# Performance work log

Measured on AMD Instinct MI355X. Metric: run time of the kernel, lower is better.

The kernel has to match this reference:

```python
import jax, jax.numpy as jnp
import numpy as np

B, H, W, C = 32, 32, 32, 256
AD, RR = 8, 16
DN = ('NHWC', 'HWIO', 'NHWC')


def _conv(a, w, dil=1, groups=1):
    return jax.lax.conv_general_dilated(a, w, (1, 1), 'SAME', rhs_dilation=(dil, dil),
                                        dimension_numbers=DN, feature_group_count=groups)


def _branch(a, w1, b1, dw, pw, b3, wd, bd):
    # (Conv1x1 + SeparableConv3x3 + DilatedConv3x3), each sigmoid-activated, averaged
    y1 = jax.nn.sigmoid(_conv(a, w1) + b1)
    y3 = jax.nn.sigmoid(_conv(_conv(a, dw, groups=a.shape[-1]), pw) + b3)  # depthwise (no bias) -> pointwise
    yd = jax.nn.sigmoid(_conv(a, wd, dil=2) + bd)
    return (y1 + y3 + yd) / 3.0


def setup_inputs() -> dict:
    key = jax.random.key(0)
    ks = iter(jax.random.split(key, 64))
    nrm = lambda shape, s=0.05: jax.random.normal(next(ks), shape, jnp.float32) * s
    d = {'x': jax.random.normal(next(ks), (B, H, W, C), jnp.float32)}
    for p in ('cc', 'ch', 'cw'):
        d[p + '1_w'] = nrm((1, 1, C, 1)); d[p + '1_b'] = jnp.zeros((1,), jnp.float32)
        d[p + '3_dw'] = nrm((3, 3, 1, C)); d[p + '3_pw'] = nrm((1, 1, C, 1)); d[p + '3_b'] = jnp.zeros((1,), jnp.float32)
        d[p + 'd_w'] = nrm((3, 3, C, 1)); d[p + 'd_b'] = jnp.zeros((1,), jnp.float32)
    d['branch_w'] = jax.random.uniform(next(ks), (3,), jnp.float32, -0.05, 0.05)
    d['d1_w'] = nrm((C, RR)); d['d1_b'] = jnp.zeros((RR,), jnp.float32)
    d['d2_w'] = nrm((RR, 1)); d['d2_b'] = jnp.zeros((1,), jnp.float32)
    for p in ('q', 'k', 'v'):
        d[p + '_w'] = nrm((1, 1, 3, AD)); d[p + '_b'] = jnp.zeros((AD,), jnp.float32)
    d['o_w'] = nrm((1, 1, AD, 1)); d['o_b'] = jnp.zeros((1,), jnp.float32)
    d['gamma'] = jnp.ones((H, W, C), jnp.float32)
    d['beta'] = jnp.zeros((H, W, C), jnp.float32)
    return d


def reference(x, cc1_w, cc1_b, cc3_dw, cc3_pw, cc3_b, ccd_w, ccd_b,
              ch1_w, ch1_b, ch3_dw, ch3_pw, ch3_b, chd_w, chd_b,
              cw1_w, cw1_b, cw3_dw, cw3_pw, cw3_b, cwd_w, cwd_b,
              branch_w, d1_w, d1_b, d2_w, d2_b,
              q_w, q_b, k_w, k_b, v_w, v_b, o_w, o_b, gamma, beta):
    Bx, Hx, Wx, Cx = x.shape
    # global SE context: GAP -> Dense(relu) -> Dense(sigmoid) -> broadcast over H,W
    g = jnp.mean(x, axis=(1, 2), keepdims=True)                       # [B,1,1,C]
    g = jax.nn.relu(g @ d1_w + d1_b)
    g = jax.nn.sigmoid(g @ d2_w + d2_b)                               # [B,1,1,1]
    # channel branch: mean over H,W -> convs over [B,1,1,C] -> scalar gate
    ca = _branch(jnp.mean(x, axis=(1, 2), keepdims=True), cc1_w, cc1_b, cc3_dw, cc3_pw, cc3_b, ccd_w, ccd_b)  # [B,1,1,1]
    x_c = x * ca
    # height branch: mean over W -> [B,1,H,C] -> convs -> [B,1,H,1] -> gate per-H
    ha_in = jnp.transpose(jnp.mean(x, axis=2, keepdims=True), (0, 2, 1, 3))
    ha = _branch(ha_in, ch1_w, ch1_b, ch3_dw, ch3_pw, ch3_b, chd_w, chd_b)
    x_h = x * jnp.transpose(ha, (0, 2, 1, 3))                         # [B,H,1,1] broadcast
    # width branch: mean over H -> [B,1,W,C] -> convs -> [B,1,W,1] -> gate per-W
    wa = _branch(jnp.mean(x, axis=1, keepdims=True), cw1_w, cw1_b, cw3_dw, cw3_pw, cw3_b, cwd_w, cwd_b)
    x_w = x * wa
    bw = jax.nn.softmax(branch_w)
    combined = bw[0] * x_c + bw[1] * x_h + bw[2] * x_w
    # small self-attention over the 3 channel-mean maps
    maps = jnp.concatenate([jnp.mean(x_c, axis=-1, keepdims=True),
                            jnp.mean(x_h, axis=-1, keepdims=True),
                            jnp.mean(x_w, axis=-1, keepdims=True)], axis=-1)  # [B,H,W,3]
    Q = (jnp.einsum('bhwc,co->bhwo', maps, q_w[0, 0]) + q_b).reshape(Bx, Hx * Wx, AD)
    K = (jnp.einsum('bhwc,co->bhwo', maps, k_w[0, 0]) + k_b).reshape(Bx, Hx * Wx, AD)
    V = (jnp.einsum('bhwc,co->bhwo', maps, v_w[0, 0]) + v_b).reshape(Bx, Hx * Wx, AD)
    att = jax.nn.softmax(jnp.einsum('bnd,bmd->bnm', Q, K) / jnp.sqrt(jnp.float32(AD)), axis=-1)
    ao = jnp.einsum('bnm,bmd->bnd', att, V).reshape(Bx, Hx, Wx, AD)
    cross = jax.nn.sigmoid(jnp.einsum('bhwd,do->bhwo', ao, o_w[0, 0]) + o_b)  # [B,H,W,1]
    y = combined * cross * g + x
    # LayerNorm over (H,W,C) per sample, keras eps=1e-3
    mu = jnp.mean(y, axis=(1, 2, 3), keepdims=True)
    var = jnp.mean((y - mu) ** 2, axis=(1, 2, 3), keepdims=True)
    return (y - mu) / jnp.sqrt(var + 1e-3) * gamma + beta
```

## Files before the change

kernel.cpp:

```cpp
#include <hip/hip_runtime.h>


#define B_   32
#define H_   32
#define W_   32
#define C_   256
#define N_   1024
#define HWC_ (32*32*256)

#define OFF_XW    0
#define OFF_XH    262144
#define OFF_MC    524288
#define OFF_M2    557056
#define OFF_T     589824
#define OFF_HA    622592
#define OFF_WA    623616
#define OFF_CA    624640
#define OFF_G     624672
#define OFF_CST   624704
#define OFF_LNP   624736
#define WS_FLOATS 628832

#if __has_builtin(__builtin_amdgcn_exp2f)
#define EXP2F(x) __builtin_amdgcn_exp2f(x)
#else
#define EXP2F(x) exp2f(x)
#endif

__device__ __forceinline__ float sigm_(float v){ return 1.f/(1.f + __expf(-v)); }
__device__ __forceinline__ float dot4_(float4 a, float4 b){
  return a.x*b.x + a.y*b.y + a.z*b.z + a.w*b.w;
}

__global__ __launch_bounds__(256) void kA(const float* __restrict__ x, float* __restrict__ ws){
  __shared__ float4 sl4[256];
  const int blk = blockIdx.x, b = blk >> 5, h = blk & 31;
  const int tid = threadIdx.x, lane = tid & 63, wv = tid >> 6;
  const float* xp = x + (size_t)blk*(W_*C_);
  float4 v[8];
  #pragma unroll
  for (int k = 0; k < 8; ++k) v[k] = ((const float4*)xp)[tid + k*256];
  #pragma unroll
  for (int k = 0; k < 8; ++k){
    float s = v[k].x + v[k].y + v[k].z + v[k].w;
    float q = v[k].x*v[k].x + v[k].y*v[k].y + v[k].z*v[k].z + v[k].w*v[k].w;
    #pragma unroll
    for (int d = 1; d < 64; d <<= 1){ s += __shfl_xor(s, d); q += __shfl_xor(q, d); }
    if (lane == 0){
      const int w = k*4 + wv;
      ws[OFF_MC + b*N_ + h*W_ + w] = s * (1.f/C_);
      ws[OFF_M2 + b*N_ + h*W_ + w] = q;
    }
  }
  float4 a = v[0];
  #pragma unroll
  for (int k = 1; k < 8; ++k){ a.x += v[k].x; a.y += v[k].y; a.z += v[k].z; a.w += v[k].w; }
  sl4[tid] = a;
  __syncthreads();
  if (tid < 64){
    const float4 p0 = sl4[tid], p1 = sl4[tid+64], p2 = sl4[tid+128], p3 = sl4[tid+192];
    float4 o;
    o.x = (p0.x+p1.x+p2.x+p3.x)*(1.f/W_);
    o.y = (p0.y+p1.y+p2.y+p3.y)*(1.f/W_);
    o.z = (p0.z+p1.z+p2.z+p3.z)*(1.f/W_);
    o.w = (p0.w+p1.w+p2.w+p3.w)*(1.f/W_);
    ((float4*)(ws + OFF_XW + (size_t)blk*C_))[tid] = o;
  }
}

__global__ __launch_bounds__(256) void kB(const float* __restrict__ x, float* __restrict__ ws){
  __shared__ float4 sl4[256];
  const int blk = blockIdx.x, b = blk >> 5, w = blk & 31;
  const int tid = threadIdx.x;
  const int hh = tid >> 6, c4 = (tid & 63)*4;
  const float* xp = x + (size_t)b*HWC_ + (size_t)w*C_ + c4;
  float4 acc = {0.f,0.f,0.f,0.f};
  #pragma unroll
  for (int hb = 0; hb < 8; ++hb){
    const int h = hb*4 + hh;
    const float4 v = *(const float4*)(xp + (size_t)h*(W_*C_));
    acc.x += v.x; acc.y += v.y; acc.z += v.z; acc.w += v.w;
  }
  sl4[tid] = acc;
  __syncthreads();
  if (tid < 64){
    const float4 a = sl4[tid], b2 = sl4[tid+64], c = sl4[tid+128], d = sl4[tid+192];
    float4 o;
    o.x = (a.x+b2.x+c.x+d.x)*(1.f/H_);
    o.y = (a.y+b2.y+c.y+d.y)*(1.f/H_);
    o.z = (a.z+b2.z+c.z+d.z)*(1.f/H_);
    o.w = (a.w+b2.w+c.w+d.w)*(1.f/H_);
    *(float4*)&ws[OFF_XH + (b*W_ + w)*C_ + tid*4] = o;
  }
}

__global__ __launch_bounds__(256) void kC(float* __restrict__ ws,
  const float* __restrict__ cc1_w, const float* __restrict__ cc1_b, const float* __restrict__ cc3_dw,
  const float* __restrict__ cc3_pw, const float* __restrict__ cc3_b, const float* __restrict__ ccd_w, const float* __restrict__ ccd_b,
  const float* __restrict__ ch1_w, const float* __restrict__ ch1_b, const float* __restrict__ ch3_dw,
  const float* __restrict__ ch3_pw, const float* __restrict__ ch3_b, const float* __restrict__ chd_w, const float* __restrict__ chd_b,
  const float* __restrict__ cw1_w, const float* __restrict__ cw1_b, const float* __restrict__ cw3_dw,
  const float* __restrict__ cw3_pw, const float* __restrict__ cw3_b, const float* __restrict__ cwd_w, const float* __restrict__ cwd_b,
  const float* __restrict__ branch_w, const float* __restrict__ d1_w, const float* __restrict__ d1_b,
  const float* __restrict__ d2_w, const float* __restrict__ d2_b,
  const float* __restrict__ q_w, const float* __restrict__ q_b, const float* __restrict__ k_w, const float* __restrict__ k_b,
  const float* __restrict__ v_w, const float* __restrict__ v_b, const float* __restrict__ o_w, const float* __restrict__ o_b)
{
  const int b = blockIdx.x, y = blockIdx.y;
  const int tid = threadIdx.x, lane = tid & 63, wv = tid >> 6;

  if (y < 16){
    const int prof = y >> 3;
    const int h = ((y & 7) << 2) | wv;
    const float* P  = ws + (prof ? OFF_XH : OFF_XW) + b*(32*C_);
    const float* w1 = prof ? cw1_w  : ch1_w;
    const float* b1 = prof ? cw1_b  : ch1_b;
    const float* dw = prof ? cw3_dw : ch3_dw;
    const float* pw = prof ? cw3_pw : ch3_pw;
    const float* b3 = prof ? cw3_b  : ch3_b;
    const float* wd = prof ? cwd_w  : chd_w;
    const float* bd = prof ? cwd_b  : chd_b;
    const int c4 = lane*4;
    const float4 z4 = {0.f,0.f,0.f,0.f};
    const float4 r0  = *(const float4*)(P + h*C_ + c4);
    const float4 rm1 = (h > 0)  ? *(const float4*)(P + (h-1)*C_ + c4) : z4;
    const float4 rp1 = (h < 31) ? *(const float4*)(P + (h+1)*C_ + c4) : z4;
    const float4 rm2 = (h > 1)  ? *(const float4*)(P + (h-2)*C_ + c4) : z4;
    const float4 rp2 = (h < 30) ? *(const float4*)(P + (h+2)*C_ + c4) : z4;
    const float4 w1q = *(const float4*)(w1 + c4);
    const float4 d3  = *(const float4*)(dw + 3*C_ + c4);
    const float4 d4  = *(const float4*)(dw + 4*C_ + c4);
    const float4 d5  = *(const float4*)(dw + 5*C_ + c4);
    const float4 pwq = *(const float4*)(pw + c4);
    const float4 g3  = *(const float4*)(wd + 3*C_ + c4);
    const float4 g4  = *(const float4*)(wd + 4*C_ + c4);
    const float4 g5  = *(const float4*)(wd + 5*C_ + c4);
    float s1 = dot4_(r0, w1q);
    float4 dv;
    dv.x = rm1.x*d3.x + r0.x*d4.x + rp1.x*d5.x;
    dv.y = rm1.y*d3.y + r0.y*d4.y + rp1.y*d5.y;
    dv.z = rm1.z*d3.z + r0.z*d4.z + rp1.z*d5.z;
    dv.w = rm1.w*d3.w + r0.w*d4.w + rp1.w*d5.w;
    float s3 = dot4_(dv, pwq);
    float sd = (rm2.x*g3.x + r0.x*g4.x + rp2.x*g5.x)
             + (rm2.y*g3.y + r0.y*g4.y + rp2.y*g5.y)
             + (rm2.z*g3.z + r0.z*g4.z + rp2.z*g5.z)
             + (rm2.w*g3.w + r0.w*g4.w + rp2.w*g5.w);
    #pragma unroll
    for (int d = 1; d < 64; d <<= 1){ s1 += __shfl_xor(s1,d); s3 += __shfl_xor(s3,d); sd += __shfl_xor(sd,d); }
    if (lane == 0)
      ws[(prof ? OFF_WA : OFF_HA) + b*32 + h] =
          (sigm_(s1 + b1[0]) + sigm_(s3 + b3[0]) + sigm_(sd + bd[0])) * (1.f/3.f);
    return;
  }

  __shared__ float gvec[C_];
  { float s = 0.f;
    const float* P = ws + OFF_XW + b*(32*C_);
    #pragma unroll
    for (int h = 0; h < H_; ++h) s += P[h*C_ + tid];
    gvec[tid] = s * (1.f/H_); }
  __syncthreads();

  if (wv == 0){
    float s1 = 0.f, s3 = 0.f, sd = 0.f;
    #pragma unroll
    for (int k = 0; k < 4; ++k){
      const int c = lane + k*64;
      const float v = gvec[c];
      s1 = fmaf(v, cc1_w[c], s1);
      s3 = fmaf(v*cc3_dw[4*C_+c], cc3_pw[c], s3);
      sd = fmaf(v, ccd_w[4*C_+c], sd);
    }
    #pragma unroll
    for (int d = 1; d < 64; d <<= 1){ s1 += __shfl_xor(s1,d); s3 += __shfl_xor(s3,d); sd += __shfl_xor(sd,d); }
    if (lane == 0)
      ws[OFF_CA + b] = (sigm_(s1+cc1_b[0]) + sigm_(s3+cc3_b[0]) + sigm_(sd+ccd_b[0])) * (1.f/3.f);
  } else if (wv == 1){
    const int r16 = lane & 15, cg = lane >> 4;
    float s = 0.f;
    #pragma unroll
    for (int i = 0; i < 64; ++i){
      const int c = cg*64 + i;
      s = fmaf(gvec[c], d1_w[c*16 + r16], s);
    }
    s += __shfl_xor(s, 16); s += __shfl_xor(s, 32);
    float t = fmaxf(s + d1_b[r16], 0.f) * d2_w[r16];
    t += __shfl_xor(t, 1); t += __shfl_xor(t, 2); t += __shfl_xor(t, 4); t += __shfl_xor(t, 8);
    if (lane == 0) ws[OFF_G + b] = sigm_(t + d2_b[0]);
  } else if (wv == 2 && b == 0){
    if (lane < 16){
      const int i = lane >> 2, j = lane & 3;
      float s = 0.f;
      #pragma unroll
      for (int d = 0; d < 8; ++d){
        const float qv = (i < 3) ? q_w[i*8+d] : q_b[d];
        const float kv = (j < 3) ? k_w[j*8+d] : k_b[d];
        s = fmaf(qv, kv, s);
      }
      ws[OFF_CST + i*4 + j] = s * 0.51010305898f;
    } else if (lane < 19){
      const int i = lane - 16;
      float s = 0.f;
      #pragma unroll
      for (int d = 0; d < 8; ++d) s = fmaf(v_w[i*8+d], o_w[d], s);
      ws[OFF_CST + lane] = s;
    } else if (lane == 19){
      float s = o_b[0];
      #pragma unroll
      for (int d = 0; d < 8; ++d) s = fmaf(v_b[d], o_w[d], s);
      ws[OFF_CST + 19] = s;
    } else if (lane == 20){
      const float b0 = branch_w[0], b1 = branch_w[1], b2 = branch_w[2];
      const float mx = fmaxf(b0, fmaxf(b1, b2));
      const float e0 = __expf(b0-mx), e1 = __expf(b1-mx), e2 = __expf(b2-mx);
      const float inv = 1.f/(e0+e1+e2);
      ws[OFF_CST+20] = e0*inv; ws[OFF_CST+21] = e1*inv; ws[OFF_CST+22] = e2*inv;
      ws[OFF_CST+23] = 0.f;
    }
  }
}

__global__ __launch_bounds__(256, 4) void kD(float* __restrict__ ws){
  __shared__ __align__(16) float mcs[N_];
  __shared__ __align__(16) float qs [N_];
  __shared__ float ha_s[32], wa_s[32], cst[24], sc[2], red[8];
  const int blk = blockIdx.x, b = blk >> 6, rblk = blk & 63;
  const int tid = threadIdx.x, lane = tid & 63, wv = tid >> 6;
  const int r = tid >> 4, sub = tid & 15;
  const int sh = sub >> 3, sw = sub & 7;
  const int n = rblk*16 + r;
  const int hn = n >> 5, wn = n & 31;

  const float4 v  = ((const float4*)(ws + OFF_MC + b*N_))[tid];
  const float m2v = ws[OFF_M2 + b*N_ + n];
  const float mcn = ws[OFF_MC + b*N_ + n];
  if (tid < 32){ ha_s[tid] = ws[OFF_HA + b*32 + tid]; wa_s[tid] = ws[OFF_WA + b*32 + tid]; }
  else if (tid >= 64 && tid < 88) cst[tid-64] = ws[OFF_CST + (tid-64)];
  else if (tid == 96){ sc[0] = ws[OFF_CA + b]; sc[1] = ws[OFF_G + b]; }
  *(float4*)&mcs[tid*4] = v;
  __syncthreads();

  const float ca = sc[0], gg = sc[1];
  {
    const int hm0 = tid >> 3;
    const int wm0 = (tid*4) & 31;
    const float base = ca*cst[16] + cst[17]*ha_s[hm0];
    float4 q;
    q.x = v.x * (base + cst[18]*wa_s[wm0+0]);
    q.y = v.y * (base + cst[18]*wa_s[wm0+1]);
    q.z = v.z * (base + cst[18]*wa_s[wm0+2]);
    q.w = v.w * (base + cst[18]*wa_s[wm0+3]);
    *(float4*)&qs[tid*4] = q;
  }
  __syncthreads();

  const float u0 = mcn*ca, u1 = mcn*ha_s[hn], u2 = mcn*wa_s[wn];
  const float p0 = u0*cst[0] + u1*cst[4] + u2*cst[8]  + cst[12];
  const float p1 = u0*cst[1] + u1*cst[5] + u2*cst[9]  + cst[13];
  const float p2 = u0*cst[2] + u1*cst[6] + u2*cst[10] + cst[14];
  const float p3 = u0*cst[3] + u1*cst[7] + u2*cst[11] + cst[15];
  const float pc = p0 * ca;

  const float4 w4 = *(const float4*)&wa_s[4*sw];
  float4 pw;
  pw.x = p2*w4.x; pw.y = p2*w4.y; pw.z = p2*w4.z; pw.w = p2*w4.w;

  float Z = 0.f, ACC = 0.f;
  #pragma unroll
  for (int i = 0; i < 16; ++i){
    const int hm = sh*16 + i;
    const float th = fmaf(p1, ha_s[hm], pc);
    const float4 m4 = *(const float4*)&mcs[hm*32 + 4*sw];
    const float4 q4 = *(const float4*)&qs [hm*32 + 4*sw];
    { const float ee = EXP2F(fmaf(m4.x, th + pw.x, p3)); Z += ee; ACC = fmaf(ee, q4.x, ACC); }
    { const float ee = EXP2F(fmaf(m4.y, th + pw.y, p3)); Z += ee; ACC = fmaf(ee, q4.y, ACC); }
    { const float ee = EXP2F(fmaf(m4.z, th + pw.z, p3)); Z += ee; ACC = fmaf(ee, q4.z, ACC); }
    { const float ee = EXP2F(fmaf(m4.w, th + pw.w, p3)); Z += ee; ACC = fmaf(ee, q4.w, ACC); }
  }
  #pragma unroll
  for (int d = 1; d < 16; d <<= 1){
    Z   += __shfl_xor(Z, d);
    ACC += __shfl_xor(ACC, d);
  }

  float t1 = 0.f, t2 = 0.f;
  if (sub == 0){
    const float dot = ACC / Z + cst[19];
    const float cross = 1.f / (1.f + __expf(-dot));
    const float S = cst[20]*ca + cst[21]*ha_s[hn] + cst[22]*wa_s[wn];
    const float T = fmaf(S*cross, gg, 1.f);
    ws[OFF_T + b*N_ + n] = T;
    t1 = T * mcn * (float)C_;
    t2 = T * T * m2v;
  }
  #pragma unroll
  for (int d = 1; d < 64; d <<= 1){ t1 += __shfl_xor(t1,d); t2 += __shfl_xor(t2,d); }
  if (lane == 0){ red[wv] = t1; red[4+wv] = t2; }
  __syncthreads();
  if (tid == 0){
    ws[OFF_LNP + (b*64 + rblk)*2 + 0] = red[0]+red[1]+red[2]+red[3];
    ws[OFF_LNP + (b*64 + rblk)*2 + 1] = red[4]+red[5]+red[6]+red[7];
  }
}

__global__ __launch_bounds__(256) void kF(const float* __restrict__ x, const float* __restrict__ gamma,
                                          const float* __restrict__ beta, const float* __restrict__ ws,
                                          float* __restrict__ out){
  const int blk = blockIdx.x, b = blk >> 5, h = blk & 31;
  const int tid = threadIdx.x;
  __shared__ float a1s[32];
  __shared__ float mu_r[2];
  if (tid < 64){
    float s1 = ws[OFF_LNP + (b*64 + tid)*2 + 0];
    float s2 = ws[OFF_LNP + (b*64 + tid)*2 + 1];
    #pragma unroll
    for (int d = 1; d < 64; d <<= 1){ s1 += __shfl_xor(s1, d); s2 += __shfl_xor(s2, d); }
    if (tid == 0){
      const float mu  = s1 * (1.f/HWC_);
      const float var = s2 * (1.f/HWC_) - mu*mu;
      const float rstd = rsqrtf(var + 1e-3f);
      mu_r[0] = mu * rstd; mu_r[1] = rstd;
    }
  }
  __syncthreads();
  if (tid < 32) a1s[tid] = ws[OFF_T + b*N_ + h*32 + tid] * mu_r[1];
  __syncthreads();
  const float murstd = mu_r[0];
  const size_t base = (size_t)(b*H_ + h)*(W_*C_);
  const float4* xp = (const float4*)(x + base);
  const float4* gp = (const float4*)(gamma + (size_t)h*(W_*C_));
  const float4* bp = (const float4*)(beta  + (size_t)h*(W_*C_));
  float4* op = (float4*)(out + base);
  #pragma unroll
  for (int k = 0; k < 8; ++k){
    const int f = tid + k*256;
    const float a1 = a1s[f >> 6];
    const float4 xv = xp[f], gv = gp[f], bv = bp[f];
    float4 o;
    o.x = fmaf(fmaf(xv.x, a1, -murstd), gv.x, bv.x);
    o.y = fmaf(fmaf(xv.y, a1, -murstd), gv.y, bv.y);
    o.z = fmaf(fmaf(xv.z, a1, -murstd), gv.z, bv.z);
    o.w = fmaf(fmaf(xv.w, a1, -murstd), gv.w, bv.w);
    op[f] = o;
  }
}

extern "C" void kernel_launch(void* const* d_in, const int* in_sizes, int n_in,
                              void* d_out, int out_size, void* d_ws, size_t ws_size,
                              hipStream_t stream){
  (void)in_sizes; (void)n_in; (void)out_size;
  if (ws_size < (size_t)WS_FLOATS * sizeof(float)) return;
  const float* x      = (const float*)d_in[0];
  const float* cc1_w  = (const float*)d_in[1];
  const float* cc1_b  = (const float*)d_in[2];
  const float* cc3_dw = (const float*)d_in[3];
  const float* cc3_pw = (const float*)d_in[4];
  const float* cc3_b  = (const float*)d_in[5];
  const float* ccd_w  = (const float*)d_in[6];
  const float* ccd_b  = (const float*)d_in[7];
  const float* ch1_w  = (const float*)d_in[8];
  const float* ch1_b  = (const float*)d_in[9];
  const float* ch3_dw = (const float*)d_in[10];
  const float* ch3_pw = (const float*)d_in[11];
  const float* ch3_b  = (const float*)d_in[12];
  const float* chd_w  = (const float*)d_in[13];
  const float* chd_b  = (const float*)d_in[14];
  const float* cw1_w  = (const float*)d_in[15];
  const float* cw1_b  = (const float*)d_in[16];
  const float* cw3_dw = (const float*)d_in[17];
  const float* cw3_pw = (const float*)d_in[18];
  const float* cw3_b  = (const float*)d_in[19];
  const float* cwd_w  = (const float*)d_in[20];
  const float* cwd_b  = (const float*)d_in[21];
  const float* branch_w = (const float*)d_in[22];
  const float* d1_w   = (const float*)d_in[23];
  const float* d1_b   = (const float*)d_in[24];
  const float* d2_w   = (const float*)d_in[25];
  const float* d2_b   = (const float*)d_in[26];
  const float* q_w    = (const float*)d_in[27];
  const float* q_b    = (const float*)d_in[28];
  const float* k_w    = (const float*)d_in[29];
  const float* k_b    = (const float*)d_in[30];
  const float* v_w    = (const float*)d_in[31];
  const float* v_b    = (const float*)d_in[32];
  const float* o_w    = (const float*)d_in[33];
  const float* o_b    = (const float*)d_in[34];
  const float* gamma  = (const float*)d_in[35];
  const float* beta   = (const float*)d_in[36];
  float* ws = (float*)d_ws;
  float* out = (float*)d_out;

  kA<<<dim3(1024), dim3(256), 0, stream>>>(x, ws);
  kB<<<dim3(1024), dim3(256), 0, stream>>>(x, ws);
  kC<<<dim3(B_, 17), dim3(256), 0, stream>>>(ws,
      cc1_w, cc1_b, cc3_dw, cc3_pw, cc3_b, ccd_w, ccd_b,
      ch1_w, ch1_b, ch3_dw, ch3_pw, ch3_b, chd_w, chd_b,
      cw1_w, cw1_b, cw3_dw, cw3_pw, cw3_b, cwd_w, cwd_b,
      branch_w, d1_w, d1_b, d2_w, d2_b,
      q_w, q_b, k_w, k_b, v_w, v_b, o_w, o_b);
  kD<<<dim3(B_*64), dim3(256), 0, stream>>>(ws);
  kF<<<dim3(B_*H_), dim3(256), 0, stream>>>(x, gamma, beta, ws, out);
}
```

Measured before the change: 46.24 us.

## Fuse row and column reductions into one pass over x with partial sums

Replaces separate row-mean and column-mean kernels, which each read all of x, with one kernel that reads each row of x once and accumulates per-group column partial sums into workspace. A small second kernel then sums the eight partials per column. This removes a full second read of the input at the cost of extra partial-sum traffic and a kernel with only 256 blocks processing rows serially, which lowers parallelism.

After: 50.39 us. 1.09x slower.

```diff
diff --git a/kernel.cpp b/kernel.cpp
--- a/kernel.cpp
+++ b/kernel.cpp
@@ -19,7 +19,8 @@
 #define OFF_G     624672
 #define OFF_CST   624704
 #define OFF_LNP   624736
-#define WS_FLOATS 628832
+#define OFF_XHP   628832
+#define WS_FLOATS 2725984
 
 #if __has_builtin(__builtin_amdgcn_exp2f)
 #define EXP2F(x) __builtin_amdgcn_exp2f(x)
@@ -32,66 +33,69 @@
   return a.x*b.x + a.y*b.y + a.z*b.z + a.w*b.w;
 }
 
-__global__ __launch_bounds__(256) void kA(const float* __restrict__ x, float* __restrict__ ws){
+__global__ __launch_bounds__(256) void kA5(const float* __restrict__ x, float* __restrict__ ws){
   __shared__ float4 sl4[256];
-  const int blk = blockIdx.x, b = blk >> 5, h = blk & 31;
+  const int blk = blockIdx.x, b = blk >> 3, hq = blk & 7;
   const int tid = threadIdx.x, lane = tid & 63, wv = tid >> 6;
-  const float* xp = x + (size_t)blk*(W_*C_);
-  float4 v[8];
-  #pragma unroll
-  for (int k = 0; k < 8; ++k) v[k] = ((const float4*)xp)[tid + k*256];
-  #pragma unroll
-  for (int k = 0; k < 8; ++k){
-    float s = v[k].x + v[k].y + v[k].z + v[k].w;
-    float q = v[k].x*v[k].x + v[k].y*v[k].y + v[k].z*v[k].z + v[k].w*v[k].w;
-    #pragma unroll
-    for (int d = 1; d < 64; d <<= 1){ s += __shfl_xor(s, d); q += __shfl_xor(q, d); }
-    if (lane == 0){
-      const int w = k*4 + wv;
-      ws[OFF_MC + b*N_ + h*W_ + w] = s * (1.f/C_);
-      ws[OFF_M2 + b*N_ + h*W_ + w] = q;
-    }
-  }
-  float4 a = v[0];
-  #pragma unroll
-  for (int k = 1; k < 8; ++k){ a.x += v[k].x; a.y += v[k].y; a.z += v[k].z; a.w += v[k].w; }
-  sl4[tid] = a;
-  __syncthreads();
-  if (tid < 64){
-    const float4 p0 = sl4[tid], p1 = sl4[tid+64], p2 = sl4[tid+128], p3 = sl4[tid+192];
-    float4 o;
-    o.x = (p0.x+p1.x+p2.x+p3.x)*(1.f/W_);
-    o.y = (p0.y+p1.y+p2.y+p3.y)*(1.f/W_);
-    o.z = (p0.z+p1.z+p2.z+p3.z)*(1.f/W_);
-    o.w = (p0.w+p1.w+p2.w+p3.w)*(1.f/W_);
-    ((float4*)(ws + OFF_XW + (size_t)blk*C_))[tid] = o;
-  }
-}
-
-__global__ __launch_bounds__(256) void kB(const float* __restrict__ x, float* __restrict__ ws){
-  __shared__ float4 sl4[256];
+  float4 colacc[8];
+  #pragma unroll
+  for (int k = 0; k < 8; ++k) colacc[k] = make_float4(0.f, 0.f, 0.f, 0.f);
+
+  #pragma unroll
+  for (int r = 0; r < 4; ++r){
+    const int h = hq*4 + r;
+    const float* xp = x + (size_t)(b*H_ + h)*(W_*C_);
+    float4 v[8];
+    #pragma unroll
+    for (int k = 0; k < 8; ++k) v[k] = ((const float4*)xp)[tid + k*256];
+    #pragma unroll
+    for (int k = 0; k < 8; ++k){
+      float s = v[k].x + v[k].y + v[k].z + v[k].w;
+      float q = v[k].x*v[k].x + v[k].y*v[k].y + v[k].z*v[k].z + v[k].w*v[k].w;
+      #pragma unroll
+      for (int d = 1; d < 64; d <<= 1){ s += __shfl_xor(s, d); q += __shfl_xor(q, d); }
+      if (lane == 0){
+        const int w = k*4 + wv;
+        ws[OFF_MC + b*N_ + h*W_ + w] = s * (1.f/C_);
+        ws[OFF_M2 + b*N_ + h*W_ + w] = q;
+      }
+    }
+    {
+      float4 a = v[0];
+      #pragma unroll
+      for (int k = 1; k < 8; ++k){ a.x += v[k].x; a.y += v[k].y; a.z += v[k].z; a.w += v[k].w; }
+      sl4[tid] = a;
+    }
+    __syncthreads();
+    if (tid < 64){
+      const float4 p0 = sl4[tid], p1 = sl4[tid+64], p2 = sl4[tid+128], p3 = sl4[tid+192];
+      float4 o;
+      o.x = (p0.x+p1.x+p2.x+p3.x)*(1.f/W_);
+      o.y = (p0.y+p1.y+p2.y+p3.y)*(1.f/W_);
+      o.z = (p0.z+p1.z+p2.z+p3.z)*(1.f/W_);
+      o.w = (p0.w+p1.w+p2.w+p3.w)*(1.f/W_);
+      ((float4*)(ws + OFF_XW + (size_t)(b*H_ + h)*C_))[tid] = o;
+    }
+    __syncthreads();
+    #pragma unroll
+    for (int k = 0; k < 8; ++k){
+      colacc[k].x += v[k].x; colacc[k].y += v[k].y;
+      colacc[k].z += v[k].z; colacc[k].w += v[k].w;
+    }
+  }
+  float4* pp = (float4*)(ws + OFF_XHP + (size_t)blk*(W_*C_));
+  #pragma unroll
+  for (int k = 0; k < 8; ++k) pp[tid + k*256] = colacc[k];
+}
+
+__global__ __launch_bounds__(256) void kB2(float* __restrict__ ws){
   const int blk = blockIdx.x, b = blk >> 5, w = blk & 31;
   const int tid = threadIdx.x;
-  const int hh = tid >> 6, c4 = (tid & 63)*4;
-  const float* xp = x + (size_t)b*HWC_ + (size_t)w*C_ + c4;
-  float4 acc = {0.f,0.f,0.f,0.f};
-  #pragma unroll
-  for (int hb = 0; hb < 8; ++hb){
-    const int h = hb*4 + hh;
-    const float4 v = *(const float4*)(xp + (size_t)h*(W_*C_));
-    acc.x += v.x; acc.y += v.y; acc.z += v.z; acc.w += v.w;
-  }
-  sl4[tid] = acc;
-  __syncthreads();
-  if (tid < 64){
-    const float4 a = sl4[tid], b2 = sl4[tid+64], c = sl4[tid+128], d = sl4[tid+192];
-    float4 o;
-    o.x = (a.x+b2.x+c.x+d.x)*(1.f/H_);
-    o.y = (a.y+b2.y+c.y+d.y)*(1.f/H_);
-    o.z = (a.z+b2.z+c.z+d.z)*(1.f/H_);
-    o.w = (a.w+b2.w+c.w+d.w)*(1.f/H_);
-    *(float4*)&ws[OFF_XH + (b*W_ + w)*C_ + tid*4] = o;
-  }
+  float s = 0.f;
+  #pragma unroll
+  for (int q = 0; q < 8; ++q)
+    s += ws[OFF_XHP + (size_t)(b*8 + q)*(W_*C_) + w*C_ + tid];
+  ws[OFF_XH + (size_t)(b*W_ + w)*C_ + tid] = s * (1.f/H_);
 }
 
 __global__ __launch_bounds__(256) void kC(float* __restrict__ ws,
@@ -391,8 +395,8 @@
   float* ws = (float*)d_ws;
   float* out = (float*)d_out;
 
-  kA<<<dim3(1024), dim3(256), 0, stream>>>(x, ws);
-  kB<<<dim3(1024), dim3(256), 0, stream>>>(x, ws);
+  kA5<<<dim3(256), dim3(256), 0, stream>>>(x, ws);
+  kB2<<<dim3(1024), dim3(256), 0, stream>>>(ws);
   kC<<<dim3(B_, 17), dim3(256), 0, stream>>>(ws,
       cc1_w, cc1_b, cc3_dw, cc3_pw, cc3_b, ccd_w, ccd_b,
       ch1_w, ch1_b, ch3_dw, ch3_pw, ch3_b, chd_w, chd_b,
```
